# Kernel optimization log

Measured on AMD Instinct MI355X. Metric: run time of the kernel, lower is better.

The kernel has to match this reference:

```python
import jax, jax.numpy as jnp
import numpy as np

B, T, KQ, KT, NDOF = 1024, 1024, 15, 20, 7


def huber(x, delta=1.0):
    ax = jnp.abs(x)
    return jnp.where(ax < delta, 0.5 * x * x, delta * (ax - 0.5 * delta))


def setup_inputs() -> dict:
    key = jax.random.key(0)
    ks = jax.random.split(key, 12)
    q_cps = jax.random.normal(ks[0], (B, KQ, NDOF), dtype=jnp.float32)
    # time-spline control points must be positive so dtau_dt > 0
    t_cps = jax.random.uniform(ks[1], (B, KT, 1), dtype=jnp.float32) + 0.5
    # B-spline basis matrices for q(tau): [1, T, KQ]
    N = jax.random.normal(ks[2], (1, T, KQ), dtype=jnp.float32)
    dN = jax.random.normal(ks[3], (1, T, KQ), dtype=jnp.float32)
    ddN = jax.random.normal(ks[4], (1, T, KQ), dtype=jnp.float32)
    dddN = jax.random.normal(ks[5], (1, T, KQ), dtype=jnp.float32)
    # time-spline basis: Nt nonnegative so dtau_dt stays positive
    Nt = jax.random.uniform(ks[6], (1, T, KT), dtype=jnp.float32)
    dNt = jax.random.normal(ks[7], (1, T, KT), dtype=jnp.float32)
    ddNt = jax.random.normal(ks[8], (1, T, KT), dtype=jnp.float32)
    q_dot_limits = jnp.array([1.4835, 1.4835, 1.7453, 1.3090, 2.2689, 2.3562, 2.3562], dtype=jnp.float32)
    q_ddot_limits = 10.0 * q_dot_limits
    q_dddot_limits = 100.0 * q_dot_limits
    torque_limits = jnp.array([320.0, 320.0, 176.0, 176.0, 110.0, 40.0, 40.0], dtype=jnp.float32)
    return {"q_cps": q_cps, "t_cps": t_cps, "N": N, "dN": dN, "ddN": ddN,
            "dddN": dddN, "Nt": Nt, "dNt": dNt, "ddNt": ddNt,
            "q_dot_limits": q_dot_limits, "q_ddot_limits": q_ddot_limits,
            "q_dddot_limits": q_dddot_limits, "torque_limits": torque_limits}


def reference(q_cps, t_cps, N, dN, ddN, dddN, Nt, dNt, ddNt,
              q_dot_limits, q_ddot_limits, q_dddot_limits, torque_limits):
    # spline evaluations: [B, T, NDOF] and [B, T, 1]
    q = jnp.einsum('ijk,lkm->ljm', N, q_cps)
    q_dot_tau = jnp.einsum('ijk,lkm->ljm', dN, q_cps)
    q_ddot_tau = jnp.einsum('ijk,lkm->ljm', ddN, q_cps)
    q_dddot_tau = jnp.einsum('ijk,lkm->ljm', dddN, q_cps)
    dtau_dt = jnp.einsum('ijk,lkm->ljm', Nt, t_cps)
    ddtau_dtt = jnp.einsum('ijk,lkm->ljm', dNt, t_cps)
    dddtau_dttt = jnp.einsum('ijk,lkm->ljm', ddNt, t_cps)

    dt = 1.0 / dtau_dt[..., 0] / dtau_dt.shape[1]  # [B, T]
    t_cumsum = jnp.cumsum(dt, axis=-1)
    t = jnp.sum(dt, axis=-1)

    dtau_dt2 = dtau_dt ** 2
    q_dot = q_dot_tau * dtau_dt
    q_ddot = q_ddot_tau * dtau_dt2 + ddtau_dtt * q_dot_tau * dtau_dt
    q_dddot = (q_dddot_tau * dtau_dt ** 3
               + 3.0 * q_ddot_tau * ddtau_dtt * dtau_dt2
               + q_dot_tau * dtau_dt2 * dddtau_dttt
               + q_dot_tau * ddtau_dtt ** 2 * dtau_dt)

    # original rnea() returns zeros as the forward torque value
    torque = jnp.zeros_like(q)

    dt_e = dt[..., None]  # [B, T, 1]
    torque_loss = jnp.sum(huber(jax.nn.relu(jnp.abs(torque) - torque_limits)) * dt_e, axis=1)
    q_dot_loss = jnp.sum(huber(jax.nn.relu(jnp.abs(q_dot) - q_dot_limits)) * dt_e, axis=1)
    q_ddot_loss = jnp.sum(huber(jax.nn.relu(jnp.abs(q_ddot) - q_ddot_limits)) * dt_e, axis=1)
    q_dddot_loss = jnp.sum(huber(jax.nn.relu(jnp.abs(q_dddot) - q_dddot_limits)) * dt_e, axis=1)

    model_losses = jnp.concatenate([q_dot_loss, q_ddot_loss, q_dddot_loss], axis=-1)
    model_loss = jnp.sum(model_losses)
    return (model_loss, q_dot_loss, q_ddot_loss, q_dddot_loss, torque_loss,
            q, q_dot, q_ddot, q_dddot, torque, t, t_cumsum, dt)
```

## Files before the change

### kernel.cpp

```cpp
#include <hip/hip_runtime.h>

#define BB 1024
#define TT 1024
#define KQ 15
#define KT 20
#define NDOF 7

#define OFF_MODEL 0
#define OFF_QDL   1
#define OFF_QDDL  (1 + BB*NDOF)
#define OFF_QDDDL (1 + 2*BB*NDOF)
#define OFF_TQL   (1 + 3*BB*NDOF)
#define OFF_Q     (1 + 4*BB*NDOF)
#define OFF_QD    (OFF_Q    + (size_t)BB*TT*NDOF)
#define OFF_QDD   (OFF_QD   + (size_t)BB*TT*NDOF)
#define OFF_QDDD  (OFF_QDD  + (size_t)BB*TT*NDOF)
#define OFF_TQ    (OFF_QDDD + (size_t)BB*TT*NDOF)
#define OFF_T     (OFF_TQ   + (size_t)BB*TT*NDOF)
#define OFF_TCUM  (OFF_T    + (size_t)BB)
#define OFF_DT    (OFF_TCUM + (size_t)BB*TT)

__device__ __forceinline__ float hub(float v, float lim) {
    float x = fabsf(v) - lim;
    x = fmaxf(x, 0.0f);
    return (x < 1.0f) ? 0.5f * x * x : (x - 0.5f);
}

__global__ __launch_bounds__(256) void feas_main(
    const float* __restrict__ q_cps, const float* __restrict__ t_cps,
    const float* __restrict__ Nb,  const float* __restrict__ dNb,
    const float* __restrict__ ddNb, const float* __restrict__ dddNb,
    const float* __restrict__ Ntb, const float* __restrict__ dNtb,
    const float* __restrict__ ddNtb,
    const float* __restrict__ qd_lim, const float* __restrict__ qdd_lim,
    const float* __restrict__ qddd_lim,
    float* __restrict__ out)
{
    const int b   = blockIdx.x;
    const int tid = threadIdx.x;

    __shared__ float cps[KQ * NDOF];
    __shared__ float tcs[KT];
    __shared__ float lim[3 * NDOF];
    __shared__ float dts[TT];
    __shared__ float seg[256];
    __shared__ float wred[4 * 21];

    if (tid < KQ * NDOF)               cps[tid]        = q_cps[(size_t)b * KQ * NDOF + tid];
    if (tid >= 128 && tid < 128 + KT)  tcs[tid - 128]  = t_cps[(size_t)b * KT + (tid - 128)];
    if (tid >= 160 && tid < 160 + NDOF) {
        int d = tid - 160;
        lim[d]          = qd_lim[d];
        lim[NDOF + d]   = qdd_lim[d];
        lim[2*NDOF + d] = qddd_lim[d];
    }
    __syncthreads();

    float lqd[NDOF], lqdd[NDOF], lqddd[NDOF];
    #pragma unroll
    for (int d = 0; d < NDOF; d++) { lqd[d] = 0.f; lqdd[d] = 0.f; lqddd[d] = 0.f; }

    #pragma unroll
    for (int i = 0; i < TT / 256; i++) {
        const int t = tid + 256 * i;

        const float* ntp   = Ntb  + (size_t)t * KT;
        const float* dntp  = dNtb + (size_t)t * KT;
        const float* ddntp = ddNtb + (size_t)t * KT;
        float dtau = 0.f, ddtau = 0.f, dddtau = 0.f;
        #pragma unroll
        for (int k = 0; k < KT; k++) {
            float c = tcs[k];
            dtau   += ntp[k]   * c;
            ddtau  += dntp[k]  * c;
            dddtau += ddntp[k] * c;
        }

        const float* np    = Nb    + (size_t)t * KQ;
        const float* dnp   = dNb   + (size_t)t * KQ;
        const float* ddnp  = ddNb  + (size_t)t * KQ;
        const float* dddnp = dddNb + (size_t)t * KQ;
        float aq[NDOF], a1[NDOF], a2[NDOF], a3[NDOF];
        #pragma unroll
        for (int d = 0; d < NDOF; d++) { aq[d] = 0.f; a1[d] = 0.f; a2[d] = 0.f; a3[d] = 0.f; }
        #pragma unroll
        for (int k = 0; k < KQ; k++) {
            float n0 = np[k], n1 = dnp[k], n2 = ddnp[k], n3 = dddnp[k];
            #pragma unroll
            for (int d = 0; d < NDOF; d++) {
                float c = cps[k * NDOF + d];
                aq[d] += n0 * c; a1[d] += n1 * c; a2[d] += n2 * c; a3[d] += n3 * c;
            }
        }

        const float dtau2 = dtau * dtau;
        const float dtau3 = dtau2 * dtau;
        const float dtv   = 1.0f / (dtau * (float)TT);
        dts[t] = dtv;
        out[OFF_DT + (size_t)b * TT + t] = dtv;

        const size_t base = ((size_t)b * TT + t) * NDOF;
        #pragma unroll
        for (int d = 0; d < NDOF; d++) {
            float qd   = a1[d] * dtau;
            float qdd  = a2[d] * dtau2 + ddtau * a1[d] * dtau;
            float qddd = a3[d] * dtau3 + 3.0f * a2[d] * ddtau * dtau2
                       + a1[d] * dtau2 * dddtau + a1[d] * ddtau * ddtau * dtau;
            out[OFF_Q    + base + d] = aq[d];
            out[OFF_QD   + base + d] = qd;
            out[OFF_QDD  + base + d] = qdd;
            out[OFF_QDDD + base + d] = qddd;
            out[OFF_TQ   + base + d] = 0.0f;
            lqd[d]   += hub(qd,   lim[d])          * dtv;
            lqdd[d]  += hub(qdd,  lim[NDOF + d])   * dtv;
            lqddd[d] += hub(qddd, lim[2*NDOF + d]) * dtv;
        }
    }
    __syncthreads();

    const int s4 = 4 * tid;
    float c0 = dts[s4];
    float c1 = c0 + dts[s4 + 1];
    float c2 = c1 + dts[s4 + 2];
    float c3 = c2 + dts[s4 + 3];
    seg[tid] = c3;
    __syncthreads();
    #pragma unroll
    for (int off = 1; off < 256; off <<= 1) {
        float v = 0.0f;
        if (tid >= off) v = seg[tid - off];
        __syncthreads();
        if (tid >= off) seg[tid] += v;
        __syncthreads();
    }
    const float excl  = (tid > 0) ? seg[tid - 1] : 0.0f;
    const float total = seg[255];
    {
        const size_t tb = OFF_TCUM + (size_t)b * TT + s4;
        out[tb + 0] = c0 + excl;
        out[tb + 1] = c1 + excl;
        out[tb + 2] = c2 + excl;
        out[tb + 3] = c3 + excl;
    }
    if (tid == 0) out[OFF_T + b] = total;
    if (tid < NDOF) out[OFF_TQL + (size_t)b * NDOF + tid] = 0.0f;

    const int lane = tid & 63;
    const int wv   = tid >> 6;
    #pragma unroll
    for (int d = 0; d < NDOF; d++) {
        float v0 = lqd[d], v1 = lqdd[d], v2 = lqddd[d];
        #pragma unroll
        for (int off = 32; off > 0; off >>= 1) {
            v0 += __shfl_down(v0, off);
            v1 += __shfl_down(v1, off);
            v2 += __shfl_down(v2, off);
        }
        if (lane == 0) {
            wred[wv * 21 + d]            = v0;
            wred[wv * 21 + NDOF + d]     = v1;
            wred[wv * 21 + 2*NDOF + d]   = v2;
        }
    }
    __syncthreads();
    if (tid < 21) {
        float s = wred[tid] + wred[21 + tid] + wred[42 + tid] + wred[63 + tid];
        int d = tid % NDOF;
        int which = tid / NDOF;
        size_t o = (which == 0) ? OFF_QDL : (which == 1) ? OFF_QDDL : OFF_QDDDL;
        out[o + (size_t)b * NDOF + d] = s;
        wred[tid] = s;
    }
    __syncthreads();
    if (tid == 0) {
        float p = 0.f;
        #pragma unroll
        for (int j = 0; j < 21; j++) p += wred[j];
        atomicAdd(out + OFF_MODEL, p);
    }
}

extern "C" void kernel_launch(void* const* d_in, const int* in_sizes, int n_in,
                              void* d_out, int out_size, void* d_ws, size_t ws_size,
                              hipStream_t stream) {
    const float* q_cps    = (const float*)d_in[0];
    const float* t_cps    = (const float*)d_in[1];
    const float* Nb       = (const float*)d_in[2];
    const float* dNb      = (const float*)d_in[3];
    const float* ddNb     = (const float*)d_in[4];
    const float* dddNb    = (const float*)d_in[5];
    const float* Ntb      = (const float*)d_in[6];
    const float* dNtb     = (const float*)d_in[7];
    const float* ddNtb    = (const float*)d_in[8];
    const float* qd_lim   = (const float*)d_in[9];
    const float* qdd_lim  = (const float*)d_in[10];
    const float* qddd_lim = (const float*)d_in[11];
    float* out = (float*)d_out;

    hipMemsetAsync(d_out, 0, sizeof(float), stream);
    feas_main<<<dim3(BB), dim3(256), 0, stream>>>(
        q_cps, t_cps, Nb, dNb, ddNb, dddNb, Ntb, dNtb, ddNtb,
        qd_lim, qdd_lim, qddd_lim, out);
}
```

Baseline: 269.2 us.

## Stage basis tiles and output rows through LDS for coalesced global access

The time loop is now processed in 256-step chunks. Each chunk's spline basis rows are loaded cooperatively into shared memory with float4 and padded-stride copies, replacing per-thread strided global reads. The q/q_dot/q_ddot/q_dddot values are written to shared memory first and then stored as contiguous coalesced runs. This targets the strided per-thread stores of 7-float records. The cost is extra barriers per chunk and control points read from global memory. The cumsum stage now re-reads dt values that the same block just wrote to global memory, which relies on block-level visibility of those writes.

```diff
diff --git a/kernel.cpp b/kernel.cpp
--- a/kernel.cpp
+++ b/kernel.cpp
@@ -5,6 +5,9 @@
 #define KQ 15
 #define KT 20
 #define NDOF 7
+#define CHK 256
+#define NCHK (TT / CHK)
+#define KTP 21
 
 #define OFF_MODEL 0
 #define OFF_QDL   1
@@ -20,6 +23,11 @@
 #define OFF_TCUM  (OFF_T    + (size_t)BB)
 #define OFF_DT    (OFF_TCUM + (size_t)BB*TT)
 
+#define QB_STR    (CHK*KQ)
+#define TB_STR    (CHK*KTP)
+#define OS_STR    (CHK*NDOF)
+#define SBUF_FL   (3*TB_STR)
+
 __device__ __forceinline__ float hub(float v, float lim) {
     float x = fabsf(v) - lim;
     x = fmaxf(x, 0.0f);
@@ -39,90 +47,138 @@
     const int b   = blockIdx.x;
     const int tid = threadIdx.x;
 
-    __shared__ float cps[KQ * NDOF];
-    __shared__ float tcs[KT];
-    __shared__ float lim[3 * NDOF];
-    __shared__ float dts[TT];
-    __shared__ float seg[256];
-    __shared__ float wred[4 * 21];
-
-    if (tid < KQ * NDOF)               cps[tid]        = q_cps[(size_t)b * KQ * NDOF + tid];
-    if (tid >= 128 && tid < 128 + KT)  tcs[tid - 128]  = t_cps[(size_t)b * KT + (tid - 128)];
-    if (tid >= 160 && tid < 160 + NDOF) {
-        int d = tid - 160;
-        lim[d]          = qd_lim[d];
-        lim[NDOF + d]   = qdd_lim[d];
-        lim[2*NDOF + d] = qddd_lim[d];
-    }
-    __syncthreads();
+    __shared__ float sbuf[SBUF_FL];
+
+    const float* cps = q_cps + (size_t)b * KQ * NDOF;
+    const float* tcp = t_cps + (size_t)b * KT;
 
     float lqd[NDOF], lqdd[NDOF], lqddd[NDOF];
     #pragma unroll
     for (int d = 0; d < NDOF; d++) { lqd[d] = 0.f; lqdd[d] = 0.f; lqddd[d] = 0.f; }
 
-    #pragma unroll
-    for (int i = 0; i < TT / 256; i++) {
-        const int t = tid + 256 * i;
-
-        const float* ntp   = Ntb  + (size_t)t * KT;
-        const float* dntp  = dNtb + (size_t)t * KT;
-        const float* ddntp = ddNtb + (size_t)t * KT;
+    #pragma unroll 1
+    for (int c = 0; c < NCHK; ++c) {
+        {
+            const float4* s0 = (const float4*)(Nb    + (size_t)c * QB_STR);
+            const float4* s1 = (const float4*)(dNb   + (size_t)c * QB_STR);
+            const float4* s2 = (const float4*)(ddNb  + (size_t)c * QB_STR);
+            const float4* s3 = (const float4*)(dddNb + (size_t)c * QB_STR);
+            float4* dst = (float4*)sbuf;
+            #pragma unroll
+            for (int j = 0; j < 4; ++j) {
+                const int idx = j * 256 + tid;
+                if (idx < QB_STR / 4) {
+                    dst[0 * (QB_STR/4) + idx] = s0[idx];
+                    dst[1 * (QB_STR/4) + idx] = s1[idx];
+                    dst[2 * (QB_STR/4) + idx] = s2[idx];
+                    dst[3 * (QB_STR/4) + idx] = s3[idx];
+                }
+            }
+        }
+        __syncthreads();
+
+        float aq[NDOF], a1[NDOF], a2[NDOF], a3[NDOF];
+        #pragma unroll
+        for (int d = 0; d < NDOF; d++) { aq[d] = 0.f; a1[d] = 0.f; a2[d] = 0.f; a3[d] = 0.f; }
+        {
+            const float* p = sbuf + tid * KQ;
+            #pragma unroll
+            for (int k = 0; k < KQ; ++k) {
+                const float n0 = p[k];
+                const float n1 = p[1 * QB_STR + k];
+                const float n2 = p[2 * QB_STR + k];
+                const float n3 = p[3 * QB_STR + k];
+                #pragma unroll
+                for (int d = 0; d < NDOF; ++d) {
+                    const float cc = cps[k * NDOF + d];
+                    aq[d] = fmaf(n0, cc, aq[d]);
+                    a1[d] = fmaf(n1, cc, a1[d]);
+                    a2[d] = fmaf(n2, cc, a2[d]);
+                    a3[d] = fmaf(n3, cc, a3[d]);
+                }
+            }
+        }
+        __syncthreads();
+
+        {
+            const float* s0 = Ntb   + (size_t)c * CHK * KT;
+            const float* s1 = dNtb  + (size_t)c * CHK * KT;
+            const float* s2 = ddNtb + (size_t)c * CHK * KT;
+            #pragma unroll 1
+            for (int j = 0; j < KT; ++j) {
+                const unsigned g = (unsigned)(j * 256 + tid);
+                const unsigned t = g / 20u;
+                const unsigned k = g - t * 20u;
+                const unsigned l = t * KTP + k;
+                sbuf[0 * TB_STR + l] = s0[g];
+                sbuf[1 * TB_STR + l] = s1[g];
+                sbuf[2 * TB_STR + l] = s2[g];
+            }
+        }
+        __syncthreads();
+
         float dtau = 0.f, ddtau = 0.f, dddtau = 0.f;
-        #pragma unroll
-        for (int k = 0; k < KT; k++) {
-            float c = tcs[k];
-            dtau   += ntp[k]   * c;
-            ddtau  += dntp[k]  * c;
-            dddtau += ddntp[k] * c;
-        }
-
-        const float* np    = Nb    + (size_t)t * KQ;
-        const float* dnp   = dNb   + (size_t)t * KQ;
-        const float* ddnp  = ddNb  + (size_t)t * KQ;
-        const float* dddnp = dddNb + (size_t)t * KQ;
-        float aq[NDOF], a1[NDOF], a2[NDOF], a3[NDOF];
-        #pragma unroll
-        for (int d = 0; d < NDOF; d++) { aq[d] = 0.f; a1[d] = 0.f; a2[d] = 0.f; a3[d] = 0.f; }
-        #pragma unroll
-        for (int k = 0; k < KQ; k++) {
-            float n0 = np[k], n1 = dnp[k], n2 = ddnp[k], n3 = dddnp[k];
-            #pragma unroll
-            for (int d = 0; d < NDOF; d++) {
-                float c = cps[k * NDOF + d];
-                aq[d] += n0 * c; a1[d] += n1 * c; a2[d] += n2 * c; a3[d] += n3 * c;
-            }
-        }
-
+        {
+            const float* p = sbuf + tid * KTP;
+            #pragma unroll
+            for (int k = 0; k < KT; ++k) {
+                const float tc = tcp[k];
+                dtau   = fmaf(p[k],              tc, dtau);
+                ddtau  = fmaf(p[1 * TB_STR + k], tc, ddtau);
+                dddtau = fmaf(p[2 * TB_STR + k], tc, dddtau);
+            }
+        }
         const float dtau2 = dtau * dtau;
         const float dtau3 = dtau2 * dtau;
         const float dtv   = 1.0f / (dtau * (float)TT);
-        dts[t] = dtv;
-        out[OFF_DT + (size_t)b * TT + t] = dtv;
-
-        const size_t base = ((size_t)b * TT + t) * NDOF;
-        #pragma unroll
-        for (int d = 0; d < NDOF; d++) {
-            float qd   = a1[d] * dtau;
-            float qdd  = a2[d] * dtau2 + ddtau * a1[d] * dtau;
-            float qddd = a3[d] * dtau3 + 3.0f * a2[d] * ddtau * dtau2
-                       + a1[d] * dtau2 * dddtau + a1[d] * ddtau * ddtau * dtau;
-            out[OFF_Q    + base + d] = aq[d];
-            out[OFF_QD   + base + d] = qd;
-            out[OFF_QDD  + base + d] = qdd;
-            out[OFF_QDDD + base + d] = qddd;
-            out[OFF_TQ   + base + d] = 0.0f;
-            lqd[d]   += hub(qd,   lim[d])          * dtv;
-            lqdd[d]  += hub(qdd,  lim[NDOF + d])   * dtv;
-            lqddd[d] += hub(qddd, lim[2*NDOF + d]) * dtv;
-        }
-    }
-    __syncthreads();
+        out[OFF_DT + (size_t)b * TT + c * CHK + tid] = dtv;
+        __syncthreads();
+
+        #pragma unroll
+        for (int d = 0; d < NDOF; ++d) {
+            const float qd   = a1[d] * dtau;
+            const float qdd  = a2[d] * dtau2 + ddtau * a1[d] * dtau;
+            const float qddd = a3[d] * dtau3 + 3.0f * a2[d] * ddtau * dtau2
+                             + a1[d] * dtau2 * dddtau + a1[d] * ddtau * ddtau * dtau;
+            const int o = tid * NDOF + d;
+            sbuf[0 * OS_STR + o] = aq[d];
+            sbuf[1 * OS_STR + o] = qd;
+            sbuf[2 * OS_STR + o] = qdd;
+            sbuf[3 * OS_STR + o] = qddd;
+            lqd[d]   += hub(qd,   qd_lim[d])   * dtv;
+            lqdd[d]  += hub(qdd,  qdd_lim[d])  * dtv;
+            lqddd[d] += hub(qddd, qddd_lim[d]) * dtv;
+        }
+        __syncthreads();
+
+        {
+            const size_t gb = (size_t)b * TT * NDOF + (size_t)c * OS_STR;
+            #pragma unroll
+            for (int j = 0; j < NDOF; ++j) {
+                const int f = j * 256 + tid;
+                out[OFF_Q    + gb + f] = sbuf[0 * OS_STR + f];
+                out[OFF_QD   + gb + f] = sbuf[1 * OS_STR + f];
+                out[OFF_QDD  + gb + f] = sbuf[2 * OS_STR + f];
+                out[OFF_QDDD + gb + f] = sbuf[3 * OS_STR + f];
+                out[OFF_TQ   + gb + f] = 0.0f;
+            }
+        }
+        __syncthreads();
+    }
 
     const int s4 = 4 * tid;
-    float c0 = dts[s4];
-    float c1 = c0 + dts[s4 + 1];
-    float c2 = c1 + dts[s4 + 2];
-    float c3 = c2 + dts[s4 + 3];
+    const size_t dtb = OFF_DT + (size_t)b * TT;
+    const float d0 = out[dtb + s4 + 0];
+    const float d1 = out[dtb + s4 + 1];
+    const float d2 = out[dtb + s4 + 2];
+    const float d3 = out[dtb + s4 + 3];
+    const float c0 = d0;
+    const float c1 = c0 + d1;
+    const float c2 = c1 + d2;
+    const float c3 = c2 + d3;
+
+    float* seg  = sbuf + 1024;
+    float* wred = sbuf + 1280;
     seg[tid] = c3;
     __syncthreads();
     #pragma unroll
@@ -135,12 +191,19 @@
     }
     const float excl  = (tid > 0) ? seg[tid - 1] : 0.0f;
     const float total = seg[255];
+
+    sbuf[s4 + 0] = c0 + excl;
+    sbuf[s4 + 1] = c1 + excl;
+    sbuf[s4 + 2] = c2 + excl;
+    sbuf[s4 + 3] = c3 + excl;
+    __syncthreads();
     {
-        const size_t tb = OFF_TCUM + (size_t)b * TT + s4;
-        out[tb + 0] = c0 + excl;
-        out[tb + 1] = c1 + excl;
-        out[tb + 2] = c2 + excl;
-        out[tb + 3] = c3 + excl;
+        const size_t tb = OFF_TCUM + (size_t)b * TT;
+        #pragma unroll
+        for (int j = 0; j < 4; ++j) {
+            const int f = j * 256 + tid;
+            out[tb + f] = sbuf[f];
+        }
     }
     if (tid == 0) out[OFF_T + b] = total;
     if (tid < NDOF) out[OFF_TQL + (size_t)b * NDOF + tid] = 0.0f;
@@ -157,17 +220,17 @@
             v2 += __shfl_down(v2, off);
         }
         if (lane == 0) {
-            wred[wv * 21 + d]            = v0;
-            wred[wv * 21 + NDOF + d]     = v1;
-            wred[wv * 21 + 2*NDOF + d]   = v2;
+            wred[wv * 21 + d]          = v0;
+            wred[wv * 21 + NDOF + d]   = v1;
+            wred[wv * 21 + 2*NDOF + d] = v2;
         }
     }
     __syncthreads();
     if (tid < 21) {
         float s = wred[tid] + wred[21 + tid] + wred[42 + tid] + wred[63 + tid];
-        int d = tid % NDOF;
-        int which = tid / NDOF;
-        size_t o = (which == 0) ? OFF_QDL : (which == 1) ? OFF_QDDL : OFF_QDDDL;
+        const int d     = tid % NDOF;
+        const int which = tid / NDOF;
+        const size_t o = (which == 0) ? (size_t)OFF_QDL : (which == 1) ? (size_t)OFF_QDDL : (size_t)OFF_QDDDL;
         out[o + (size_t)b * NDOF + d] = s;
         wred[tid] = s;
     }
```

Measured after the change: 283.1 us. 5.2% more time.
